# Kernel tuning notes

Measured on AMD Instinct MI355X. Metric: run time of the kernel, lower is better.

## Reference

```python
import jax, jax.numpy as jnp
import numpy as np

B, T, C, H = 2, 2048, 1024, 16
HD = C // H  # head_dim = 64

def _rope(x, cos, sin):
    # x: [B,H,T,HD]; cos/sin: [T,HD//2]
    x2 = x.reshape(*x.shape[:-1], HD // 2, 2)
    x0, x1 = x2[..., 0], x2[..., 1]
    # complex multiply (x0 + i x1) * (cos + i sin)
    o0 = x0 * cos - x1 * sin
    o1 = x0 * sin + x1 * cos
    return jnp.stack([o0, o1], axis=-1).reshape(x.shape)

def setup_inputs() -> dict:
    key = jax.random.key(0)
    k1, k2, k3 = jax.random.split(key, 3)
    x = jax.random.normal(k1, (B, T, C), dtype=jnp.float32)
    w_qkv = jax.random.normal(k2, (C, 3 * C), dtype=jnp.float32) * (1.0 / np.sqrt(C))
    w_proj = jax.random.normal(k3, (C, C), dtype=jnp.float32) * (1.0 / np.sqrt(C))
    # standard RoPE frequencies: theta_j = 10000^(-2j/HD), angles t*theta_j
    inv_freq = 1.0 / (10000.0 ** (np.arange(0, HD, 2, dtype=np.float32) / HD))  # [HD//2]
    ang = np.arange(T, dtype=np.float32)[:, None] * inv_freq[None, :]           # [T,HD//2]
    return {"x": x, "w_qkv": w_qkv, "w_proj": w_proj,
            "freqs_cos": jnp.asarray(np.cos(ang)), "freqs_sin": jnp.asarray(np.sin(ang))}

def reference(x, w_qkv, w_proj, freqs_cos, freqs_sin):
    qkv = x @ w_qkv                                   # [B,T,3C]
    q, k, v = jnp.split(qkv, 3, axis=-1)
    def heads(t):
        return t.reshape(B, T, H, HD).transpose(0, 2, 1, 3)  # [B,H,T,HD]
    q, k, v = heads(q), heads(k), heads(v)
    q = _rope(q, freqs_cos, freqs_sin)
    k = _rope(k, freqs_cos, freqs_sin)
    scores = jnp.einsum('bhqd,bhkd->bhqk', q, k) * (1.0 / np.sqrt(HD))
    causal = jnp.tril(jnp.ones((T, T), dtype=bool))
    scores = jnp.where(causal, scores, jnp.finfo(scores.dtype).min)
    attn = jax.nn.softmax(scores, axis=-1)
    y = jnp.einsum('bhqk,bhkd->bhqd', attn, v)        # [B,H,T,HD]
    y = y.transpose(0, 2, 1, 3).reshape(B, T, C)
    return y @ w_proj
```

## Files before the change

kernel.cpp:

```cpp
#include <hip/hip_runtime.h>

typedef float  floatx4 __attribute__((ext_vector_type(4)));
typedef _Float16 half8 __attribute__((ext_vector_type(8)));
typedef _Float16 half4v __attribute__((ext_vector_type(4)));

__device__ __forceinline__ void gld16(const void* g, void* l) {
    __builtin_amdgcn_global_load_lds(
        (const __attribute__((address_space(1))) void*)g,
        (__attribute__((address_space(3))) void*)l, 16, 0, 0);
}

__global__ __launch_bounds__(256) void conv_x_kernel(const float* __restrict__ x,
                                                     _Float16* __restrict__ xh) {
    int i = blockIdx.x * 256 + threadIdx.x;
    float4 v = ((const float4*)x)[i];
    half4v o = { (_Float16)v.x, (_Float16)v.y, (_Float16)v.z, (_Float16)v.w };
    ((half4v*)xh)[i] = o;
}

__global__ __launch_bounds__(256) void transpose_f32f16(const float* __restrict__ W,
                                                        _Float16* __restrict__ WT,
                                                        int K, int N) {
    __shared__ _Float16 t[64][72];
    int n0 = blockIdx.x * 64, k0 = blockIdx.y * 64;
    int c = threadIdx.x & 63, r4 = threadIdx.x >> 6;
    for (int rr = 0; rr < 64; rr += 4) {
        int k = k0 + rr + r4;
        t[rr + r4][c] = (_Float16)W[(size_t)k * N + n0 + c];
    }
    __syncthreads();
    for (int rr = 0; rr < 64; rr += 4) {
        int n = n0 + rr + r4;
        WT[(size_t)n * K + k0 + c] = t[c][rr + r4];
    }
}

__global__ __launch_bounds__(256) void gemm_tn(const _Float16* __restrict__ A,
                                               const _Float16* __restrict__ BT,
                                               _Float16* __restrict__ Cf16,
                                               int M, int N, int K) {
    __shared__ __align__(16) _Float16 sAB[2 * 128 * 64];
    _Float16* sA = sAB;
    _Float16* sB = sAB + 128 * 64;

    const int tid  = threadIdx.x;
    const int wave = tid >> 6, lane = tid & 63;
    const int lrow = lane & 15, quad = lane >> 4;
    const int bm = blockIdx.x * 128, bn = blockIdx.y * 128;
    const int waveM = (wave >> 1) * 64, waveN = (wave & 1) * 64;

    floatx4 acc[4][4] = {};

    int srow[4], sccg[4];
#pragma unroll
    for (int hlf = 0; hlf < 4; ++hlf) {
        int s = tid + hlf * 256;
        srow[hlf] = s >> 3;
        sccg[hlf] = ((s & 7) ^ (srow[hlf] & 7)) * 8;
    }

    for (int k0 = 0; k0 < K; k0 += 64) {
#pragma unroll
        for (int hlf = 0; hlf < 4; ++hlf) {
            int s = tid + hlf * 256;
            gld16(A + (size_t)(bm + srow[hlf]) * K + k0 + sccg[hlf], sA + s * 8);
            gld16(BT + (size_t)(bn + srow[hlf]) * K + k0 + sccg[hlf], sB + s * 8);
        }
        __syncthreads();

#pragma unroll
        for (int kk = 0; kk < 2; ++kk) {
            half8 aF[4], bF[4];
#pragma unroll
            for (int mt = 0; mt < 4; ++mt)
                aF[mt] = *(const half8*)&sA[(waveM + mt * 16 + lrow) * 64 +
                                            (((kk * 4 + quad) ^ (lrow & 7)) * 8)];
#pragma unroll
            for (int nt = 0; nt < 4; ++nt)
                bF[nt] = *(const half8*)&sB[(waveN + nt * 16 + lrow) * 64 +
                                            (((kk * 4 + quad) ^ (lrow & 7)) * 8)];
#pragma unroll
            for (int mt = 0; mt < 4; ++mt)
#pragma unroll
                for (int nt = 0; nt < 4; ++nt)
                    acc[mt][nt] = __builtin_amdgcn_mfma_f32_16x16x32_f16(
                        aF[mt], bF[nt], acc[mt][nt], 0, 0, 0);
        }
        __syncthreads();
    }

    _Float16* ep = sAB + wave * 1152;
    const int erow = lane >> 3, ecol = (lane & 7) * 8;
#pragma unroll
    for (int mt = 0; mt < 4; ++mt) {
#pragma unroll
        for (int nt = 0; nt < 4; ++nt)
#pragma unroll
            for (int r = 0; r < 4; ++r)
                ep[(quad * 4 + r) * 72 + nt * 16 + lrow] = (_Float16)acc[mt][nt][r];
        __builtin_amdgcn_wave_barrier();
#pragma unroll
        for (int st = 0; st < 2; ++st) {
            uint4 d = *(const uint4*)&ep[(st * 8 + erow) * 72 + ecol];
            *(uint4*)&Cf16[(size_t)(bm + waveM + mt * 16 + st * 8 + erow) * N +
                           bn + waveN + ecol] = d;
        }
        __builtin_amdgcn_wave_barrier();
    }
}

__global__ __launch_bounds__(256) void gemm_tn64(const _Float16* __restrict__ A,
                                                 const _Float16* __restrict__ BT,
                                                 float* __restrict__ C,
                                                 int M, int N, int K) {
    __shared__ __align__(16) _Float16 sA[64 * 32];
    __shared__ __align__(16) _Float16 sB[128 * 32];

    const int tid  = threadIdx.x;
    const int wave = tid >> 6, lane = tid & 63;
    const int lrow = lane & 15, quad = lane >> 4;
    const int bm = blockIdx.x * 64, bn = blockIdx.y * 128;
    const int waveM = (wave >> 1) * 32, waveN = (wave & 1) * 64;

    floatx4 acc[2][4] = {};

    const int raA = tid >> 2, ccA = (((tid & 3) ^ ((tid >> 2) & 3))) * 8;
    int rB[2], cB[2];
#pragma unroll
    for (int hlf = 0; hlf < 2; ++hlf) {
        int s = tid + hlf * 256;
        rB[hlf] = s >> 2;
        cB[hlf] = ((s & 3) ^ ((s >> 2) & 3)) * 8;
    }

    for (int k0 = 0; k0 < K; k0 += 32) {
        gld16(A + (size_t)(bm + raA) * K + k0 + ccA, sA + tid * 8);
#pragma unroll
        for (int hlf = 0; hlf < 2; ++hlf) {
            int s = tid + hlf * 256;
            gld16(BT + (size_t)(bn + rB[hlf]) * K + k0 + cB[hlf], sB + s * 8);
        }
        __syncthreads();

        half8 aF[2], bF[4];
#pragma unroll
        for (int mt = 0; mt < 2; ++mt)
            aF[mt] = *(const half8*)&sA[(waveM + mt * 16 + lrow) * 32 +
                                        ((quad ^ (lrow & 3)) * 8)];
#pragma unroll
        for (int nt = 0; nt < 4; ++nt)
            bF[nt] = *(const half8*)&sB[(waveN + nt * 16 + lrow) * 32 +
                                        ((quad ^ (lrow & 3)) * 8)];
#pragma unroll
        for (int mt = 0; mt < 2; ++mt)
#pragma unroll
            for (int nt = 0; nt < 4; ++nt)
                acc[mt][nt] = __builtin_amdgcn_mfma_f32_16x16x32_f16(
                    aF[mt], bF[nt], acc[mt][nt], 0, 0, 0);
        __syncthreads();
    }

#pragma unroll
    for (int mt = 0; mt < 2; ++mt)
#pragma unroll
        for (int nt = 0; nt < 4; ++nt)
#pragma unroll
            for (int r = 0; r < 4; ++r) {
                int row = bm + waveM + mt * 16 + quad * 4 + r;
                int col = bn + waveN + nt * 16 + lrow;
                C[(size_t)row * N + col] = acc[mt][nt][r];
            }
}

__global__ __launch_bounds__(256) void rope_vt(const _Float16* __restrict__ qkv,
                                               const float* __restrict__ fc,
                                               const float* __restrict__ fs,
                                               _Float16* __restrict__ qh,
                                               _Float16* __restrict__ kh,
                                               _Float16* __restrict__ vt) {
    __shared__ _Float16 s[64][72];
    const int bh = blockIdx.y, b = bh >> 4, h = bh & 15;
    const int t0 = blockIdx.x * 64;
    const int tid = threadIdx.x;

    {
        int c4 = (tid & 15) * 4;
        int j0 = c4 >> 1;
        int rr = tid >> 4;
#pragma unroll
        for (int pass = 0; pass < 4; ++pass) {
            int tt = t0 + pass * 16 + rr;
            const _Float16* src = qkv + (size_t)(b * 2048 + tt) * 3072 + h * 64 + c4;
            float c0 = fc[tt * 32 + j0],     s0 = fs[tt * 32 + j0];
            float c1 = fc[tt * 32 + j0 + 1], s1 = fs[tt * 32 + j0 + 1];
            half4v qv = *(const half4v*)(src);
            half4v kv = *(const half4v*)(src + 1024);
            half4v qo, ko;
            {
                float x0 = (float)qv[0], x1 = (float)qv[1];
                qo[0] = (_Float16)(x0 * c0 - x1 * s0); qo[1] = (_Float16)(x0 * s0 + x1 * c0);
                x0 = (float)qv[2]; x1 = (float)qv[3];
                qo[2] = (_Float16)(x0 * c1 - x1 * s1); qo[3] = (_Float16)(x0 * s1 + x1 * c1);
                x0 = (float)kv[0]; x1 = (float)kv[1];
                ko[0] = (_Float16)(x0 * c0 - x1 * s0); ko[1] = (_Float16)(x0 * s0 + x1 * c0);
                x0 = (float)kv[2]; x1 = (float)kv[3];
                ko[2] = (_Float16)(x0 * c1 - x1 * s1); ko[3] = (_Float16)(x0 * s1 + x1 * c1);
            }
            size_t o = ((size_t)bh * 2048 + tt) * 64 + c4;
            *(half4v*)&qh[o] = qo;
            *(half4v*)&kh[o] = ko;
        }
    }
    {
        int c = tid & 63, r4 = tid >> 6;
        const _Float16* srcv = qkv + 2048 + h * 64;
        for (int rr = 0; rr < 64; rr += 4)
            s[rr + r4][c] = srcv[(size_t)(b * 2048 + t0 + rr + r4) * 3072 + c];
        __syncthreads();
        for (int rr = 0; rr < 64; rr += 4)
            vt[((size_t)bh * 64 + rr + r4) * 2048 + t0 + c] = s[c][rr + r4];
    }
}

#define U_(qc,k0,k1,dir,slot) ((qc)|((k0)<<5)|((k1)<<11)|((dir)<<17)|((slot)<<18))
__device__ const unsigned int UTAB[24] = {
    U_(15, 0,15,0,14), U_(15,16,31,0,15), U_( 7, 0,15,1, 0),
    U_(14, 0,14,0,12), U_(14,15,29,0,13),
    U_(13, 0,13,0,10), U_(13,14,27,0,11), U_( 6, 0,13,1, 0),
    U_(12, 0,12,0, 8), U_(12,13,25,0, 9),
    U_(11, 0,11,0, 6), U_(11,12,23,0, 7), U_( 5, 0,11,1, 0),
    U_(10, 0,10,0, 4), U_(10,11,21,0, 5),
    U_( 9, 0, 9,0, 2), U_( 9,10,19,0, 3), U_( 4, 0, 9,1, 0),
    U_( 8, 0, 8,0, 0), U_( 8, 9,17,0, 1),
    U_( 3, 0, 7,1, 0), U_( 2, 0, 5,1, 0), U_( 1, 0, 3,1, 0), U_( 0, 0, 1,1, 0)
};

__global__ __launch_bounds__(256, 3) void attn_sk2(const _Float16* __restrict__ Q,
                                                   const _Float16* __restrict__ Kk,
                                                   const _Float16* __restrict__ Vt,
                                                   _Float16* __restrict__ Y,
                                                   _Float16* __restrict__ Opart,
                                                   float* __restrict__ lpart) {
    __shared__ __align__(16) _Float16 sK[64 * 64];
    __shared__ __align__(16) _Float16 sV[64 * 64];
    __shared__ __align__(16) _Float16 sP[128 * 72];

    const int bh = blockIdx.x, b = bh >> 4, h = bh & 15;
    const unsigned e = UTAB[blockIdx.y];
    const int qc = e & 31, k0 = (e >> 5) & 63, k1 = (e >> 11) & 63;
    const int dir = (e >> 17) & 1, slot = (e >> 18) & 15;
    const int d0 = 2 * qc, d1 = 2 * qc + 1;

    const int tid = threadIdx.x;
    const int wave = tid >> 6, lane = tid & 63;
    const int lq = lane & 15, quad = lane >> 4;

    const _Float16* Kbase = Kk + (size_t)bh * 2048 * 64;
    const _Float16* Vbase = Vt + (size_t)bh * 64 * 2048;

    const _Float16 qscale = (_Float16)(0.125f * 1.44269504f);
    half8 qF[2][2];
#pragma unroll
    for (int g = 0; g < 2; ++g) {
        const _Float16* Qp = Q + ((size_t)bh * 2048 + qc * 128 + g * 64 + wave * 16 + lq) * 64;
#pragma unroll
        for (int ks = 0; ks < 2; ++ks)
            qF[g][ks] = (*(const half8*)(Qp + ks * 32 + quad * 8)) * qscale;
    }

    floatx4 O0[4] = {}, O1[4] = {};
    float lacc0 = 0.f, lacc1 = 0.f;

    for (int kt = k0; kt <= k1; ++kt) {
        const bool live0 = (kt <= d0);
        const _Float16* kb = Kbase + (size_t)kt * 64 * 64;
        const _Float16* vb = Vbase + kt * 64;
#pragma unroll
        for (int hlf = 0; hlf < 2; ++hlf) {
            int s = tid + hlf * 256;
            int row = s >> 3;
            int ccg = (s & 7) ^ (row & 7);
            gld16(kb + row * 64 + ccg * 8, sK + s * 8);
            gld16(vb + (size_t)row * 2048 + ccg * 8, sV + s * 8);
        }
        __syncthreads();

        half4v P0[4], P1[4];
#pragma unroll
        for (int kt4 = 0; kt4 < 4; ++kt4) {
            half8 kf0 = *(const half8*)&sK[(kt4 * 16 + lq) * 64 + ((quad ^ (lq & 7)) * 8)];
            half8 kf1 = *(const half8*)&sK[(kt4 * 16 + lq) * 64 + (((4 + quad) ^ (lq & 7)) * 8)];
            floatx4 s1 = { -12.f, -12.f, -12.f, -12.f };
            s1 = __builtin_amdgcn_mfma_f32_16x16x32_f16(kf0, qF[1][0], s1, 0, 0, 0);
            s1 = __builtin_amdgcn_mfma_f32_16x16x32_f16(kf1, qF[1][1], s1, 0, 0, 0);
            if (kt == d1) {
#pragma unroll
                for (int r = 0; r < 4; ++r)
                    if (kt4 * 16 + quad * 4 + r > wave * 16 + lq) s1[r] = -1e30f;
            }
#pragma unroll
            for (int r = 0; r < 4; ++r) s1[r] = __builtin_amdgcn_exp2f(s1[r]);
            lacc1 += s1[0] + s1[1] + s1[2] + s1[3];
            P1[kt4] = half4v{ (_Float16)s1[0], (_Float16)s1[1],
                              (_Float16)s1[2], (_Float16)s1[3] };
            if (live0) {
                floatx4 s0 = { -12.f, -12.f, -12.f, -12.f };
                s0 = __builtin_amdgcn_mfma_f32_16x16x32_f16(kf0, qF[0][0], s0, 0, 0, 0);
                s0 = __builtin_amdgcn_mfma_f32_16x16x32_f16(kf1, qF[0][1], s0, 0, 0, 0);
                if (kt == d0) {
#pragma unroll
                    for (int r = 0; r < 4; ++r)
                        if (kt4 * 16 + quad * 4 + r > wave * 16 + lq) s0[r] = -1e30f;
                }
#pragma unroll
                for (int r = 0; r < 4; ++r) s0[r] = __builtin_amdgcn_exp2f(s0[r]);
                lacc0 += s0[0] + s0[1] + s0[2] + s0[3];
                P0[kt4] = half4v{ (_Float16)s0[0], (_Float16)s0[1],
                                  (_Float16)s0[2], (_Float16)s0[3] };
            }
        }

        _Float16* pw1 = &sP[(64 + wave * 16 + lq) * 72];
#pragma unroll
        for (int kt4 = 0; kt4 < 4; ++kt4)
            *(half4v*)(pw1 + kt4 * 16 + quad * 4) = P1[kt4];
        _Float16* pw0 = &sP[(wave * 16 + lq) * 72];
        if (live0) {
#pragma unroll
            for (int kt4 = 0; kt4 < 4; ++kt4)
                *(half4v*)(pw0 + kt4 * 16 + quad * 4) = P0[kt4];
        }
        __builtin_amdgcn_wave_barrier();

        half8 aP0[2], aP1[2];
#pragma unroll
        for (int ks = 0; ks < 2; ++ks) {
            aP1[ks] = *(const half8*)(pw1 + ks * 32 + quad * 8);
            if (live0) aP0[ks] = *(const half8*)(pw0 + ks * 32 + quad * 8);
        }
#pragma unroll
        for (int nt = 0; nt < 4; ++nt)
#pragma unroll
            for (int ks = 0; ks < 2; ++ks) {
                half8 vf = *(const half8*)&sV[(nt * 16 + lq) * 64 +
                                              (((ks * 4 + quad) ^ (lq & 7)) * 8)];
                O1[nt] = __builtin_amdgcn_mfma_f32_16x16x32_f16(aP1[ks], vf, O1[nt], 0, 0, 0);
                if (live0)
                    O0[nt] = __builtin_amdgcn_mfma_f32_16x16x32_f16(aP0[ks], vf, O0[nt], 0, 0, 0);
            }
        __syncthreads();
    }

#pragma unroll
    for (int g = 0; g < 2; ++g) {
        float l = g ? lacc1 : lacc0;
        l += __shfl_xor(l, 16);
        l += __shfl_xor(l, 32);
        floatx4* O = g ? O1 : O0;
        if (dir) {
            float invl = 1.0f / l;
#pragma unroll
            for (int r = 0; r < 4; ++r) {
                float iv = __shfl(invl, (lane & 48) | (quad * 4 + r));
                int q = qc * 128 + g * 64 + wave * 16 + quad * 4 + r;
                size_t rowoff = ((size_t)b * 2048 + q) * 1024 + h * 64;
#pragma unroll
                for (int nt = 0; nt < 4; ++nt)
                    Y[rowoff + nt * 16 + lq] = (_Float16)(O[nt][r] * iv);
            }
        } else {
            int gslot = bh * 16 + slot;
            _Float16* op = Opart + (size_t)gslot * 8192;
#pragma unroll
            for (int r = 0; r < 4; ++r) {
                int row = g * 64 + wave * 16 + quad * 4 + r;
#pragma unroll
                for (int nt = 0; nt < 4; ++nt)
                    op[row * 64 + nt * 16 + lq] = (_Float16)O[nt][r];
            }
            if (quad == 0)
                lpart[gslot * 128 + g * 64 + wave * 16 + lq] = l;
        }
    }
}

__global__ __launch_bounds__(256) void attn_reduce2(const _Float16* __restrict__ Opart,
                                                    const float* __restrict__ lpart,
                                                    _Float16* __restrict__ Y) {
    const int bh = blockIdx.x, b = bh >> 4, h = bh & 15;
    const int qcx = blockIdx.y, qc = 8 + qcx;
    const int g0 = bh * 16 + qcx * 2, g1 = g0 + 1;
    const int tid = threadIdx.x;

#pragma unroll
    for (int it = 0; it < 2; ++it) {
        int idx = tid + it * 256;
        int row = idx >> 2, cs = (idx & 3) * 16;
        const _Float16* p0 = Opart + (size_t)g0 * 8192 + row * 64 + cs;
        const _Float16* p1 = Opart + (size_t)g1 * 8192 + row * 64 + cs;
        float invl = 1.0f / (lpart[g0 * 128 + row] + lpart[g1 * 128 + row]);
        half8 a0 = *(const half8*)p0, a1 = *(const half8*)(p0 + 8);
        half8 b0 = *(const half8*)p1, b1 = *(const half8*)(p1 + 8);
        half8 o0, o1;
#pragma unroll
        for (int i = 0; i < 8; ++i) {
            o0[i] = (_Float16)(((float)a0[i] + (float)b0[i]) * invl);
            o1[i] = (_Float16)(((float)a1[i] + (float)b1[i]) * invl);
        }
        _Float16* y = Y + ((size_t)b * 2048 + qc * 128 + row) * 1024 + h * 64 + cs;
        *(half8*)y = o0;
        *(half8*)(y + 8) = o1;
    }
}

extern "C" void kernel_launch(void* const* d_in, const int* in_sizes, int n_in,
                              void* d_out, int out_size, void* d_ws, size_t ws_size,
                              hipStream_t stream) {
    const float* x     = (const float*)d_in[0];
    const float* wqkv  = (const float*)d_in[1];
    const float* wproj = (const float*)d_in[2];
    const float* fc    = (const float*)d_in[3];
    const float* fs    = (const float*)d_in[4];
    float* out = (float*)d_out;

    char* ws = (char*)d_ws;
    _Float16* xh    = (_Float16*)(ws);
    _Float16* wqT   = (_Float16*)(ws + ((size_t)8  << 20));
    _Float16* wpT   = (_Float16*)(ws + ((size_t)14 << 20));
    _Float16* qkvh  = (_Float16*)(ws + ((size_t)16 << 20));
    _Float16* qh    = (_Float16*)(ws + ((size_t)40 << 20));
    _Float16* kh    = (_Float16*)(ws + ((size_t)48 << 20));
    _Float16* vt    = (_Float16*)(ws + ((size_t)56 << 20));
    _Float16* yh    = xh;
    _Float16* Opart = qkvh;
    float*    lpartf= (float*)(ws + ((size_t)26 << 20));

    conv_x_kernel<<<4096, 256, 0, stream>>>(x, xh);
    transpose_f32f16<<<dim3(48, 16), 256, 0, stream>>>(wqkv, wqT, 1024, 3072);
    transpose_f32f16<<<dim3(16, 16), 256, 0, stream>>>(wproj, wpT, 1024, 1024);
    gemm_tn<<<dim3(32, 24), 256, 0, stream>>>(xh, wqT, qkvh, 4096, 3072, 1024);
    rope_vt<<<dim3(32, 32), 256, 0, stream>>>(qkvh, fc, fs, qh, kh, vt);
    attn_sk2<<<dim3(32, 24), 256, 0, stream>>>(qh, kh, vt, yh, Opart, lpartf);
    attn_reduce2<<<dim3(32, 8), 256, 0, stream>>>(Opart, lpartf, yh);
    gemm_tn64<<<dim3(64, 8), 256, 0, stream>>>(yh, wpT, out, 4096, 1024, 1024);
}
```

Before: 186.9 us.

## Fuse RoPE and head-major scatter into QKV GEMM epilogue, slim V transpose

The QKV GEMM epilogue now applies RoPE to the Q and K sections and writes Q, K and V directly in [B,H,T,HD] layout. This replaces the separate rope_vt pass that reread the full qkv buffer. A smaller kernel now only transposes V from the head-major buffer. The aim is to cut one full read/write round trip of Q and K through global memory. In exchange the GEMM epilogue gains extra loads of the cos/sin tables and some arithmetic, and the workspace layout is rearranged.

Measured after the change: 192.9 us. 1.03x slower.

```diff
diff --git a/kernel.cpp b/kernel.cpp
--- a/kernel.cpp
+++ b/kernel.cpp
@@ -35,10 +35,14 @@
     }
 }
 
-__global__ __launch_bounds__(256) void gemm_tn(const _Float16* __restrict__ A,
-                                               const _Float16* __restrict__ BT,
-                                               _Float16* __restrict__ Cf16,
-                                               int M, int N, int K) {
+__global__ __launch_bounds__(256) void gemm_qkv(const _Float16* __restrict__ A,
+                                                const _Float16* __restrict__ BT,
+                                                const float* __restrict__ fc,
+                                                const float* __restrict__ fs,
+                                                _Float16* __restrict__ qh,
+                                                _Float16* __restrict__ kh,
+                                                _Float16* __restrict__ vh) {
+    const int K = 1024, NHALF = 64;
     __shared__ __align__(16) _Float16 sAB[2 * 128 * 64];
     _Float16* sA = sAB;
     _Float16* sB = sAB + 128 * 64;
@@ -49,6 +53,11 @@
     const int bm = blockIdx.x * 128, bn = blockIdx.y * 128;
     const int waveM = (wave >> 1) * 64, waveN = (wave & 1) * 64;
 
+    const int section = bn >> 10;
+    const int head_base = (bn & 1023) >> 6;
+    _Float16* __restrict__ D = (section == 0) ? qh : (section == 1) ? kh : vh;
+    const bool dorope = (section < 2);
+
     floatx4 acc[4][4] = {};
 
     int srow[4], sccg[4];
@@ -91,6 +100,8 @@
 
     _Float16* ep = sAB + wave * 1152;
     const int erow = lane >> 3, ecol = (lane & 7) * 8;
+    const int cc = waveN + ecol;
+    const int h = head_base + (cc >> 6), hd = cc & 63, j0 = hd >> 1;
 #pragma unroll
     for (int mt = 0; mt < 4; ++mt) {
 #pragma unroll
@@ -101,9 +112,29 @@
         __builtin_amdgcn_wave_barrier();
 #pragma unroll
         for (int st = 0; st < 2; ++st) {
-            uint4 d = *(const uint4*)&ep[(st * 8 + erow) * 72 + ecol];
-            *(uint4*)&Cf16[(size_t)(bm + waveM + mt * 16 + st * 8 + erow) * N +
-                           bn + waveN + ecol] = d;
+            int m = bm + waveM + mt * 16 + st * 8 + erow;
+            int b = m >> 11, t = m & 2047;
+            half8 v = *(const half8*)&ep[(st * 8 + erow) * 72 + ecol];
+            if (dorope) {
+                float4 c4 = *(const float4*)&fc[t * 32 + j0];
+                float4 s4 = *(const float4*)&fs[t * 32 + j0];
+                half8 o;
+                float x0, x1;
+                x0 = (float)v[0]; x1 = (float)v[1];
+                o[0] = (_Float16)(x0 * c4.x - x1 * s4.x);
+                o[1] = (_Float16)(x0 * s4.x + x1 * c4.x);
+                x0 = (float)v[2]; x1 = (float)v[3];
+                o[2] = (_Float16)(x0 * c4.y - x1 * s4.y);
+                o[3] = (_Float16)(x0 * s4.y + x1 * c4.y);
+                x0 = (float)v[4]; x1 = (float)v[5];
+                o[4] = (_Float16)(x0 * c4.z - x1 * s4.z);
+                o[5] = (_Float16)(x0 * s4.z + x1 * c4.z);
+                x0 = (float)v[6]; x1 = (float)v[7];
+                o[6] = (_Float16)(x0 * c4.w - x1 * s4.w);
+                o[7] = (_Float16)(x0 * s4.w + x1 * c4.w);
+                v = o;
+            }
+            *(half8*)&D[(((size_t)(b * 16 + h) * 2048 + t) * NHALF) + hd] = v;
         }
         __builtin_amdgcn_wave_barrier();
     }
@@ -172,54 +203,18 @@
             }
 }
 
-__global__ __launch_bounds__(256) void rope_vt(const _Float16* __restrict__ qkv,
-                                               const float* __restrict__ fc,
-                                               const float* __restrict__ fs,
-                                               _Float16* __restrict__ qh,
-                                               _Float16* __restrict__ kh,
-                                               _Float16* __restrict__ vt) {
+__global__ __launch_bounds__(256) void vtrans(const _Float16* __restrict__ vh,
+                                              _Float16* __restrict__ vt) {
     __shared__ _Float16 s[64][72];
-    const int bh = blockIdx.y, b = bh >> 4, h = bh & 15;
-    const int t0 = blockIdx.x * 64;
+    const int bh = blockIdx.y, t0 = blockIdx.x * 64;
     const int tid = threadIdx.x;
-
-    {
-        int c4 = (tid & 15) * 4;
-        int j0 = c4 >> 1;
-        int rr = tid >> 4;
-#pragma unroll
-        for (int pass = 0; pass < 4; ++pass) {
-            int tt = t0 + pass * 16 + rr;
-            const _Float16* src = qkv + (size_t)(b * 2048 + tt) * 3072 + h * 64 + c4;
-            float c0 = fc[tt * 32 + j0],     s0 = fs[tt * 32 + j0];
-            float c1 = fc[tt * 32 + j0 + 1], s1 = fs[tt * 32 + j0 + 1];
-            half4v qv = *(const half4v*)(src);
-            half4v kv = *(const half4v*)(src + 1024);
-            half4v qo, ko;
-            {
-                float x0 = (float)qv[0], x1 = (float)qv[1];
-                qo[0] = (_Float16)(x0 * c0 - x1 * s0); qo[1] = (_Float16)(x0 * s0 + x1 * c0);
-                x0 = (float)qv[2]; x1 = (float)qv[3];
-                qo[2] = (_Float16)(x0 * c1 - x1 * s1); qo[3] = (_Float16)(x0 * s1 + x1 * c1);
-                x0 = (float)kv[0]; x1 = (float)kv[1];
-                ko[0] = (_Float16)(x0 * c0 - x1 * s0); ko[1] = (_Float16)(x0 * s0 + x1 * c0);
-                x0 = (float)kv[2]; x1 = (float)kv[3];
-                ko[2] = (_Float16)(x0 * c1 - x1 * s1); ko[3] = (_Float16)(x0 * s1 + x1 * c1);
-            }
-            size_t o = ((size_t)bh * 2048 + tt) * 64 + c4;
-            *(half4v*)&qh[o] = qo;
-            *(half4v*)&kh[o] = ko;
-        }
-    }
-    {
-        int c = tid & 63, r4 = tid >> 6;
-        const _Float16* srcv = qkv + 2048 + h * 64;
-        for (int rr = 0; rr < 64; rr += 4)
-            s[rr + r4][c] = srcv[(size_t)(b * 2048 + t0 + rr + r4) * 3072 + c];
-        __syncthreads();
-        for (int rr = 0; rr < 64; rr += 4)
-            vt[((size_t)bh * 64 + rr + r4) * 2048 + t0 + c] = s[c][rr + r4];
-    }
+    int c = tid & 63, r4 = tid >> 6;
+    const _Float16* src = vh + ((size_t)bh * 2048 + t0) * 64;
+    for (int rr = 0; rr < 64; rr += 4)
+        s[rr + r4][c] = src[(size_t)(rr + r4) * 64 + c];
+    __syncthreads();
+    for (int rr = 0; rr < 64; rr += 4)
+        vt[((size_t)bh * 64 + rr + r4) * 2048 + t0 + c] = s[c][rr + r4];
 }
 
 #define U_(qc,k0,k1,dir,slot) ((qc)|((k0)<<5)|((k1)<<11)|((dir)<<17)|((slot)<<18))
@@ -427,19 +422,19 @@
     _Float16* xh    = (_Float16*)(ws);
     _Float16* wqT   = (_Float16*)(ws + ((size_t)8  << 20));
     _Float16* wpT   = (_Float16*)(ws + ((size_t)14 << 20));
-    _Float16* qkvh  = (_Float16*)(ws + ((size_t)16 << 20));
+    _Float16* vh    = (_Float16*)(ws + ((size_t)16 << 20));
+    _Float16* Opart = (_Float16*)(ws + ((size_t)24 << 20));
+    float*    lpartf= (float*)(ws + ((size_t)33 << 20));
     _Float16* qh    = (_Float16*)(ws + ((size_t)40 << 20));
     _Float16* kh    = (_Float16*)(ws + ((size_t)48 << 20));
     _Float16* vt    = (_Float16*)(ws + ((size_t)56 << 20));
     _Float16* yh    = xh;
-    _Float16* Opart = qkvh;
-    float*    lpartf= (float*)(ws + ((size_t)26 << 20));
 
     conv_x_kernel<<<4096, 256, 0, stream>>>(x, xh);
     transpose_f32f16<<<dim3(48, 16), 256, 0, stream>>>(wqkv, wqT, 1024, 3072);
     transpose_f32f16<<<dim3(16, 16), 256, 0, stream>>>(wproj, wpT, 1024, 1024);
-    gemm_tn<<<dim3(32, 24), 256, 0, stream>>>(xh, wqT, qkvh, 4096, 3072, 1024);
-    rope_vt<<<dim3(32, 32), 256, 0, stream>>>(qkvh, fc, fs, qh, kh, vt);
+    gemm_qkv<<<dim3(32, 24), 256, 0, stream>>>(xh, wqT, fc, fs, qh, kh, vh);
+    vtrans<<<dim3(32, 32), 256, 0, stream>>>(vh, vt);
     attn_sk2<<<dim3(32, 24), 256, 0, stream>>>(qh, kh, vt, yh, Opart, lpartf);
     attn_reduce2<<<dim3(32, 8), 256, 0, stream>>>(Opart, lpartf, yh);
     gemm_tn64<<<dim3(64, 8), 256, 0, stream>>>(yh, wpT, out, 4096, 1024, 1024);
```

## Merge prep kernels into one launch and use 8-wave blocks for both GEMMs

Applied to the files above, without the earlier changes.

The x conversion and the two weight transposes are combined into one `prep` kernel, dispatched by block index, which removes two launches. Both GEMM kernels move from 4 to 8 waves per block while keeping the same tile sizes. Each wave now computes half as many output subtiles, so register use per wave drops and more waves are available to hide latency. In exchange, each wave does fewer MFMAs for every LDS fragment it loads, which raises LDS read traffic per FLOP.

Measured after the change: 186.3 us. No clear change (-0.3%).

```diff
diff --git a/kernel.cpp b/kernel.cpp
--- a/kernel.cpp
+++ b/kernel.cpp
@@ -10,32 +10,38 @@
         (__attribute__((address_space(3))) void*)l, 16, 0, 0);
 }
 
-__global__ __launch_bounds__(256) void conv_x_kernel(const float* __restrict__ x,
-                                                     _Float16* __restrict__ xh) {
-    int i = blockIdx.x * 256 + threadIdx.x;
-    float4 v = ((const float4*)x)[i];
-    half4v o = { (_Float16)v.x, (_Float16)v.y, (_Float16)v.z, (_Float16)v.w };
-    ((half4v*)xh)[i] = o;
-}
-
-__global__ __launch_bounds__(256) void transpose_f32f16(const float* __restrict__ W,
-                                                        _Float16* __restrict__ WT,
-                                                        int K, int N) {
+__global__ __launch_bounds__(256) void prep(const float* __restrict__ x,
+                                            const float* __restrict__ wqkv,
+                                            const float* __restrict__ wproj,
+                                            _Float16* __restrict__ xh,
+                                            _Float16* __restrict__ wqT,
+                                            _Float16* __restrict__ wpT) {
     __shared__ _Float16 t[64][72];
-    int n0 = blockIdx.x * 64, k0 = blockIdx.y * 64;
-    int c = threadIdx.x & 63, r4 = threadIdx.x >> 6;
-    for (int rr = 0; rr < 64; rr += 4) {
-        int k = k0 + rr + r4;
-        t[rr + r4][c] = (_Float16)W[(size_t)k * N + n0 + c];
-    }
+    const int bid = blockIdx.x, tid = threadIdx.x;
+    if (bid < 4096) {
+        int i = bid * 256 + tid;
+        float4 v = ((const float4*)x)[i];
+        half4v o = { (_Float16)v.x, (_Float16)v.y, (_Float16)v.z, (_Float16)v.w };
+        ((half4v*)xh)[i] = o;
+        return;
+    }
+    const float* W; _Float16* WT; int K, N, n0, k0;
+    if (bid < 4096 + 768) {
+        int q = bid - 4096; W = wqkv; WT = wqT; K = 1024; N = 3072;
+        n0 = (q % 48) * 64; k0 = (q / 48) * 64;
+    } else {
+        int q = bid - 4864; W = wproj; WT = wpT; K = 1024; N = 1024;
+        n0 = (q % 16) * 64; k0 = (q / 16) * 64;
+    }
+    int c = tid & 63, r4 = tid >> 6;
+    for (int rr = 0; rr < 64; rr += 4)
+        t[rr + r4][c] = (_Float16)W[(size_t)(k0 + rr + r4) * N + n0 + c];
     __syncthreads();
-    for (int rr = 0; rr < 64; rr += 4) {
-        int n = n0 + rr + r4;
-        WT[(size_t)n * K + k0 + c] = t[c][rr + r4];
-    }
-}
-
-__global__ __launch_bounds__(256) void gemm_tn(const _Float16* __restrict__ A,
+    for (int rr = 0; rr < 64; rr += 4)
+        WT[(size_t)(n0 + rr + r4) * K + k0 + c] = t[c][rr + r4];
+}
+
+__global__ __launch_bounds__(512) void gemm_tn(const _Float16* __restrict__ A,
                                                const _Float16* __restrict__ BT,
                                                _Float16* __restrict__ Cf16,
                                                int M, int N, int K) {
@@ -47,22 +53,22 @@
     const int wave = tid >> 6, lane = tid & 63;
     const int lrow = lane & 15, quad = lane >> 4;
     const int bm = blockIdx.x * 128, bn = blockIdx.y * 128;
-    const int waveM = (wave >> 1) * 64, waveN = (wave & 1) * 64;
-
-    floatx4 acc[4][4] = {};
-
-    int srow[4], sccg[4];
-#pragma unroll
-    for (int hlf = 0; hlf < 4; ++hlf) {
-        int s = tid + hlf * 256;
+    const int waveM = (wave >> 2) * 64, waveN = (wave & 3) * 32;
+
+    floatx4 acc[4][2] = {};
+
+    int srow[2], sccg[2];
+#pragma unroll
+    for (int hlf = 0; hlf < 2; ++hlf) {
+        int s = tid + hlf * 512;
         srow[hlf] = s >> 3;
         sccg[hlf] = ((s & 7) ^ (srow[hlf] & 7)) * 8;
     }
 
     for (int k0 = 0; k0 < K; k0 += 64) {
 #pragma unroll
-        for (int hlf = 0; hlf < 4; ++hlf) {
-            int s = tid + hlf * 256;
+        for (int hlf = 0; hlf < 2; ++hlf) {
+            int s = tid + hlf * 512;
             gld16(A + (size_t)(bm + srow[hlf]) * K + k0 + sccg[hlf], sA + s * 8);
             gld16(BT + (size_t)(bn + srow[hlf]) * K + k0 + sccg[hlf], sB + s * 8);
         }
@@ -70,46 +76,45 @@
 
 #pragma unroll
         for (int kk = 0; kk < 2; ++kk) {
-            half8 aF[4], bF[4];
+            half8 aF[4], bF[2];
 #pragma unroll
             for (int mt = 0; mt < 4; ++mt)
                 aF[mt] = *(const half8*)&sA[(waveM + mt * 16 + lrow) * 64 +
                                             (((kk * 4 + quad) ^ (lrow & 7)) * 8)];
 #pragma unroll
-            for (int nt = 0; nt < 4; ++nt)
+            for (int nt = 0; nt < 2; ++nt)
                 bF[nt] = *(const half8*)&sB[(waveN + nt * 16 + lrow) * 64 +
                                             (((kk * 4 + quad) ^ (lrow & 7)) * 8)];
 #pragma unroll
             for (int mt = 0; mt < 4; ++mt)
 #pragma unroll
-                for (int nt = 0; nt < 4; ++nt)
+                for (int nt = 0; nt < 2; ++nt)
                     acc[mt][nt] = __builtin_amdgcn_mfma_f32_16x16x32_f16(
                         aF[mt], bF[nt], acc[mt][nt], 0, 0, 0);
         }
         __syncthreads();
     }
 
-    _Float16* ep = sAB + wave * 1152;
-    const int erow = lane >> 3, ecol = (lane & 7) * 8;
+    _Float16* ep = sAB + wave * 576;
+    const int erow = lane >> 2, ecol = (lane & 3) * 8;
 #pragma unroll
     for (int mt = 0; mt < 4; ++mt) {
 #pragma unroll
-        for (int nt = 0; nt < 4; ++nt)
+        for (int nt = 0; nt < 2; ++nt)
 #pragma unroll
             for (int r = 0; r < 4; ++r)
-                ep[(quad * 4 + r) * 72 + nt * 16 + lrow] = (_Float16)acc[mt][nt][r];
+                ep[(quad * 4 + r) * 36 + nt * 16 + lrow] = (_Float16)acc[mt][nt][r];
         __builtin_amdgcn_wave_barrier();
-#pragma unroll
-        for (int st = 0; st < 2; ++st) {
-            uint4 d = *(const uint4*)&ep[(st * 8 + erow) * 72 + ecol];
-            *(uint4*)&Cf16[(size_t)(bm + waveM + mt * 16 + st * 8 + erow) * N +
+        {
+            uint4 d = *(const uint4*)&ep[erow * 36 + ecol];
+            *(uint4*)&Cf16[(size_t)(bm + waveM + mt * 16 + erow) * N +
                            bn + waveN + ecol] = d;
         }
         __builtin_amdgcn_wave_barrier();
     }
 }
 
-__global__ __launch_bounds__(256) void gemm_tn64(const _Float16* __restrict__ A,
+__global__ __launch_bounds__(512) void gemm_tn64(const _Float16* __restrict__ A,
                                                  const _Float16* __restrict__ BT,
                                                  float* __restrict__ C,
                                                  int M, int N, int K) {
@@ -120,41 +125,32 @@
     const int wave = tid >> 6, lane = tid & 63;
     const int lrow = lane & 15, quad = lane >> 4;
     const int bm = blockIdx.x * 64, bn = blockIdx.y * 128;
-    const int waveM = (wave >> 1) * 32, waveN = (wave & 1) * 64;
-
-    floatx4 acc[2][4] = {};
-
-    const int raA = tid >> 2, ccA = (((tid & 3) ^ ((tid >> 2) & 3))) * 8;
-    int rB[2], cB[2];
-#pragma unroll
-    for (int hlf = 0; hlf < 2; ++hlf) {
-        int s = tid + hlf * 256;
-        rB[hlf] = s >> 2;
-        cB[hlf] = ((s & 3) ^ ((s >> 2) & 3)) * 8;
-    }
+    const int waveM = (wave >> 2) * 32, waveN = (wave & 3) * 32;
+
+    floatx4 acc[2][2] = {};
+
+    const int rA = tid >> 2, cA = (((tid & 3) ^ ((tid >> 2) & 3))) * 8;
+    const int rB = tid >> 2, cB = (((tid & 3) ^ ((tid >> 2) & 3))) * 8;
 
     for (int k0 = 0; k0 < K; k0 += 32) {
-        gld16(A + (size_t)(bm + raA) * K + k0 + ccA, sA + tid * 8);
-#pragma unroll
-        for (int hlf = 0; hlf < 2; ++hlf) {
-            int s = tid + hlf * 256;
-            gld16(BT + (size_t)(bn + rB[hlf]) * K + k0 + cB[hlf], sB + s * 8);
-        }
-        __syncthreads();
-
-        half8 aF[2], bF[4];
+        if (tid < 256)
+            gld16(A + (size_t)(bm + rA) * K + k0 + cA, sA + tid * 8);
+        gld16(BT + (size_t)(bn + rB) * K + k0 + cB, sB + tid * 8);
+        __syncthreads();
+
+        half8 aF[2], bF[2];
 #pragma unroll
         for (int mt = 0; mt < 2; ++mt)
             aF[mt] = *(const half8*)&sA[(waveM + mt * 16 + lrow) * 32 +
                                         ((quad ^ (lrow & 3)) * 8)];
 #pragma unroll
-        for (int nt = 0; nt < 4; ++nt)
+        for (int nt = 0; nt < 2; ++nt)
             bF[nt] = *(const half8*)&sB[(waveN + nt * 16 + lrow) * 32 +
                                         ((quad ^ (lrow & 3)) * 8)];
 #pragma unroll
         for (int mt = 0; mt < 2; ++mt)
 #pragma unroll
-            for (int nt = 0; nt < 4; ++nt)
+            for (int nt = 0; nt < 2; ++nt)
                 acc[mt][nt] = __builtin_amdgcn_mfma_f32_16x16x32_f16(
                     aF[mt], bF[nt], acc[mt][nt], 0, 0, 0);
         __syncthreads();
@@ -163,7 +159,7 @@
 #pragma unroll
     for (int mt = 0; mt < 2; ++mt)
 #pragma unroll
-        for (int nt = 0; nt < 4; ++nt)
+        for (int nt = 0; nt < 2; ++nt)
 #pragma unroll
             for (int r = 0; r < 4; ++r) {
                 int row = bm + waveM + mt * 16 + quad * 4 + r;
@@ -435,12 +431,10 @@
     _Float16* Opart = qkvh;
     float*    lpartf= (float*)(ws + ((size_t)26 << 20));
 
-    conv_x_kernel<<<4096, 256, 0, stream>>>(x, xh);
-    transpose_f32f16<<<dim3(48, 16), 256, 0, stream>>>(wqkv, wqT, 1024, 3072);
-    transpose_f32f16<<<dim3(16, 16), 256, 0, stream>>>(wproj, wpT, 1024, 1024);
-    gemm_tn<<<dim3(32, 24), 256, 0, stream>>>(xh, wqT, qkvh, 4096, 3072, 1024);
+    prep<<<5120, 256, 0, stream>>>(x, wqkv, wproj, xh, wqT, wpT);
+    gemm_tn<<<dim3(32, 24), 512, 0, stream>>>(xh, wqT, qkvh, 4096, 3072, 1024);
     rope_vt<<<dim3(32, 32), 256, 0, stream>>>(qkvh, fc, fs, qh, kh, vt);
     attn_sk2<<<dim3(32, 24), 256, 0, stream>>>(qh, kh, vt, yh, Opart, lpartf);
     attn_reduce2<<<dim3(32, 8), 256, 0, stream>>>(Opart, lpartf, yh);
-    gemm_tn64<<<dim3(64, 8), 256, 0, stream>>>(yh, wpT, out, 4096, 1024, 1024);
-}
+    gemm_tn64<<<dim3(64, 8), 512, 0, stream>>>(yh, wpT, out, 4096, 1024, 1024);
+}
```
